# Kernel tuning notes

Measured on AMD Instinct MI355X. Metric: run time of the kernel, lower is better.

## Reference

```python
import jax, jax.numpy as jnp
import numpy as np

B, TC, TP = 2, 1024, 512
NVC, NVP = 8, 4
D, K, H, DFF, L, HOR, NQ = 128, 3, 8, 512, 2, 96, 3
DK = D // H
MASK_VAL = -1e4  # finite stand-in for -inf; entmax15 support never reaches entries this far below the row max


def entmax15(z):
    # Exact 1.5-entmax over the last axis (Peters & Martins sort-based algorithm).
    z = z / 2.0
    z = z - jnp.max(z, axis=-1, keepdims=True)
    zs = jnp.flip(jnp.sort(z, axis=-1), axis=-1)  # descending
    kk = jnp.arange(1, z.shape[-1] + 1, dtype=z.dtype)
    mean = jnp.cumsum(zs, axis=-1) / kk
    meansq = jnp.cumsum(zs * zs, axis=-1) / kk
    ss = kk * (meansq - mean * mean)
    delta = (1.0 - ss) / kk
    pos = delta > 0
    sqrt_d = jnp.where(pos, jnp.sqrt(jnp.where(pos, delta, 1.0)), 0.0)  # grad-safe sqrt
    tau = mean - sqrt_d
    support = jnp.sum((tau <= zs).astype(jnp.int32), axis=-1, keepdims=True)
    tau_star = jnp.take_along_axis(tau, support - 1, axis=-1)
    return jnp.square(jnp.clip(z - tau_star, 0.0, None))


def layer_norm(x, g, b, eps=1e-5):
    m = jnp.mean(x, axis=-1, keepdims=True)
    v = jnp.mean(jnp.square(x - m), axis=-1, keepdims=True)
    return (x - m) * jax.lax.rsqrt(v + eps) * g + b


def selector(x, conv_w, conv_b, sel_w, sel_b, key):
    # x: [B, T, nv]; causal depthwise-grouped conv -> per-var local states [B, T, nv, D]
    Bs, T, nv = x.shape
    xc = jnp.transpose(x, (0, 2, 1))  # [B, nv, T]
    out = jax.lax.conv_general_dilated(
        xc, conv_w, window_strides=(1,), padding=[(K - 1, 0)],
        dimension_numbers=('NCH', 'OIH', 'NCH'), feature_group_count=nv)
    ls = out.reshape(Bs, nv, D, T) + conv_b[None, :, :, None]
    ls = jnp.transpose(ls, (0, 3, 1, 2))  # [B, T, nv, D]
    scores = ls @ sel_w + sel_b  # [B, T, nv]
    scores = jnp.clip(scores, -10.0, 10.0)
    scores = scores + 1e-4 * jax.random.normal(key, scores.shape, scores.dtype)
    w = entmax15(scores)  # [B, T, nv]
    weighted = jnp.sum(ls * w[..., None], axis=2)  # [B, T, D]
    return weighted, w


def attn_block(x, Wq, bq, Wk, bk, Wv, bv, Wo, bo):
    Bs, T, _ = x.shape
    q = (x @ Wq + bq).reshape(Bs, T, H, DK)
    k = (x @ Wk + bk).reshape(Bs, T, H, DK)
    v = (x @ Wv + bv).reshape(Bs, T, H, DK)
    scores = jnp.einsum('bthd,bshd->bhts', q, k) / jnp.sqrt(jnp.float32(DK))
    mask = jnp.triu(jnp.ones((T, T), bool), 1)
    scores = jnp.where(mask[None, None], MASK_VAL, scores)
    w = entmax15(scores)            # [B, H, T, T]
    w_avg = jnp.mean(w, axis=1)     # [B, T, T]
    v_comb = jnp.mean(v, axis=2)    # [B, T, DK]
    out = jnp.einsum('bts,bsd->btd', w_avg, v_comb)
    return out @ Wo + bo, w_avg


def forward(x_cond, x_pred, cw_c, cb_c, sw_c, sb_c, cw_p, cb_p, sw_p, sb_p,
            Wq, bq, Wk, bk, Wv, bv, Wo, bo, ln1_g, ln1_b,
            fw1, fb1, fw2, fb2, ln2_g, ln2_b, proj_w, proj_b):
    nk = jax.random.key(42)
    xc, v_cond = selector(x_cond, cw_c, cb_c, sw_c, sb_c, jax.random.fold_in(nk, 0))
    xp, v_pred = selector(x_pred, cw_p, cb_p, sw_p, sb_p, jax.random.fold_in(nk, 1))
    x = jnp.concatenate([xc, xp], axis=1)  # [B, TC+TP, D]
    logs = []
    for l in range(L):
        a, w = attn_block(x, Wq[l], bq[l], Wk[l], bk[l], Wv[l], bv[l], Wo[l], bo[l])
        x = layer_norm(x + a, ln1_g[l], ln1_b[l])
        h = jax.nn.relu(x @ fw1[l] + fb1[l])
        x = layer_norm(h @ fw2[l] + fb2[l] + x, ln2_g[l], ln2_b[l])
        logs.append(w)
    seq_last = x[:, -1, :]
    out = jnp.einsum('bd,qdh->bqh', seq_last, proj_w) + proj_b  # [B, NQ, HOR]
    return out, v_cond, v_pred, jnp.stack(logs)


def setup_inputs():
    key = jax.random.key(0)
    ks = jax.random.split(key, 16)
    def w(i, shp):
        return (0.02 * jax.random.normal(ks[i], shp)).astype(jnp.float32)
    z = lambda shp: jnp.zeros(shp, jnp.float32)
    o = lambda shp: jnp.ones(shp, jnp.float32)
    return {
        'x_cond': jax.random.normal(ks[0], (B, TC, NVC), jnp.float32),
        'x_pred': jax.random.normal(ks[1], (B, TP, NVP), jnp.float32),
        'cw_c': w(2, (NVC * D, 1, K)), 'cb_c': z((NVC, D)),
        'sw_c': w(3, (D,)), 'sb_c': z((1,)),
        'cw_p': w(4, (NVP * D, 1, K)), 'cb_p': z((NVP, D)),
        'sw_p': w(5, (D,)), 'sb_p': z((1,)),
        'Wq': w(6, (L, D, D)), 'bq': z((L, D)),
        'Wk': w(7, (L, D, D)), 'bk': z((L, D)),
        'Wv': w(8, (L, D, D)), 'bv': z((L, D)),
        'Wo': w(9, (L, DK, D)), 'bo': z((L, D)),
        'ln1_g': o((L, D)), 'ln1_b': z((L, D)),
        'fw1': w(10, (L, D, DFF)), 'fb1': z((L, DFF)),
        'fw2': w(11, (L, DFF, D)), 'fb2': z((L, D)),
        'ln2_g': o((L, D)), 'ln2_b': z((L, D)),
        'proj_w': w(12, (NQ, D, HOR)), 'proj_b': z((NQ, HOR)),
    }


def reference(x_cond, x_pred, cw_c, cb_c, sw_c, sb_c, cw_p, cb_p, sw_p, sb_p,
              Wq, bq, Wk, bk, Wv, bv, Wo, bo, ln1_g, ln1_b,
              fw1, fb1, fw2, fb2, ln2_g, ln2_b, proj_w, proj_b):
    return forward(x_cond, x_pred, cw_c, cb_c, sw_c, sb_c, cw_p, cb_p, sw_p, sb_p,
                   Wq, bq, Wk, bk, Wv, bv, Wo, bo, ln1_g, ln1_b,
                   fw1, fb1, fw2, fb2, ln2_g, ln2_b, proj_w, proj_b)
```

## Files before the change

### kernel.cpp

```cpp
#include <hip/hip_runtime.h>

namespace {

constexpr int NB_  = 2;
constexpr int TC_  = 1024;
constexpr int TP_  = 512;
constexpr int TT_  = 1536;
constexpr int D_   = 128;
constexpr int H_   = 8;
constexpr int DK_  = 16;
constexpr int DFF_ = 512;
constexpr int L_   = 2;
constexpr int HOR_ = 96;
constexpr int NQ_  = 3;

constexpr int SCP_ = TT_ + 8;

typedef _Float16 h2 __attribute__((ext_vector_type(2)));

constexpr int OFF_OUT  = 0;
constexpr int OFF_VC   = NB_ * NQ_ * HOR_;
constexpr int OFF_VP   = OFF_VC + NB_ * TC_ * 8;
constexpr int OFF_LOGS = OFF_VP + NB_ * TP_ * 4;

constexpr int WS_XA  = 0;
constexpr int WS_XB  = WS_XA  + NB_ * TT_ * D_;
constexpr int WS_Q16 = WS_XB  + NB_ * TT_ * D_;
constexpr int WS_K16 = WS_Q16 + NB_ * TT_ * D_ / 2;
constexpr int WS_VC  = WS_K16 + NB_ * TT_ * D_ / 2;
constexpr int WS_WVC = WS_VC  + NB_ * TT_ * DK_;
constexpr int WS_BVC = WS_WVC + L_ * D_ * DK_;

__device__ inline float dot2f(h2 a, h2 b, float c) {
#if __has_builtin(__builtin_amdgcn_fdot2)
    return __builtin_amdgcn_fdot2(a, b, c, false);
#else
    return c + (float)a[0] * (float)b[0] + (float)a[1] * (float)b[1];
#endif
}

__device__ inline unsigned pack2h(float a, float b) {
#if __has_builtin(__builtin_amdgcn_cvt_pkrtz)
    return __builtin_bit_cast(unsigned, __builtin_amdgcn_cvt_pkrtz(a, b));
#else
    h2 p; p[0] = (_Float16)a; p[1] = (_Float16)b;
    return __builtin_bit_cast(unsigned, p);
#endif
}

__device__ inline float fast_rcp(float x) {
#if __has_builtin(__builtin_amdgcn_rcpf)
    return __builtin_amdgcn_rcpf(x);
#else
    return 1.0f / x;
#endif
}

template <int CTRL>
__device__ inline float dpp_add(float x) {
    const int y = __builtin_amdgcn_update_dpp(
        0, __builtin_bit_cast(int, x), CTRL, 0xF, 0xF, true);
    return x + __builtin_bit_cast(float, y);
}
template <int CTRL>
__device__ inline float dpp_maxf(float x) {
    const int y = __builtin_amdgcn_update_dpp(
        __builtin_bit_cast(int, x), __builtin_bit_cast(int, x),
        CTRL, 0xF, 0xF, false);
    return fmaxf(x, __builtin_bit_cast(float, y));
}
__device__ inline float bcast63(float x) {
    return __builtin_bit_cast(float,
        __builtin_amdgcn_readlane(__builtin_bit_cast(int, x), 63));
}
__device__ inline float wave_sum_l63(float x) {
    x = dpp_add<0x111>(x); x = dpp_add<0x112>(x); x = dpp_add<0x114>(x);
    x = dpp_add<0x118>(x); x = dpp_add<0x142>(x); x = dpp_add<0x143>(x);
    return x;
}
__device__ inline float wave_sum(float x) { return bcast63(wave_sum_l63(x)); }
__device__ inline float wave_max(float x) {
    x = dpp_maxf<0x111>(x); x = dpp_maxf<0x112>(x); x = dpp_maxf<0x114>(x);
    x = dpp_maxf<0x118>(x); x = dpp_maxf<0x142>(x); x = dpp_maxf<0x143>(x);
    return bcast63(x);
}

__global__ __launch_bounds__(128) void prep_wvc_kernel(
    const float* __restrict__ Wv, const float* __restrict__ bv,
    float* __restrict__ wvc, float* __restrict__ bvc)
{
    const int l = blockIdx.x;
    const float* W  = Wv + (long)l * D_ * D_;
    const float* bb = bv + l * D_;
    float* wv = wvc + l * D_ * DK_;
    float* bo = bvc + l * DK_;
    const int tid = threadIdx.x;
    for (int idx = tid; idx < D_ * DK_; idx += 128) {
        const int i = idx >> 4, dk = idx & 15;
        float s = 0.f;
        #pragma unroll
        for (int hh = 0; hh < H_; ++hh) s += W[i * D_ + hh * DK_ + dk];
        wv[idx] = s * 0.125f;
    }
    if (tid < DK_) {
        float s = 0.f;
        #pragma unroll
        for (int hh = 0; hh < H_; ++hh) s += bb[hh * DK_ + tid];
        bo[tid] = s * 0.125f;
    }
}

template <int NV>
__device__ inline void selector_qkv_body(
    const float* __restrict__ x, const float* __restrict__ cw,
    const float* __restrict__ cb, const float* __restrict__ sw,
    const float* __restrict__ sb, float* __restrict__ vout,
    float* __restrict__ xout, int Tsel, int row_off, int blk,
    const float* __restrict__ Wq, const float* __restrict__ bq,
    const float* __restrict__ Wk, const float* __restrict__ bk,
    const float* __restrict__ wvc, const float* __restrict__ bvc,
    _Float16* __restrict__ q16, _Float16* __restrict__ k16,
    float* __restrict__ vc)
{
    const int b = blk / Tsel;
    const int t = blk - b * Tsel;
    const int tid = threadIdx.x;
    const int d = tid & 127;
    const int hi = tid >> 7;
    const int lane = tid & 63, wave = tid >> 6;

    __shared__ float wsum[4][NV];
    __shared__ float wls[NV];
    __shared__ float xr[D_];
    __shared__ float vred[DK_][8];

    float xw[3 * NV];
    #pragma unroll
    for (int kk = 0; kk < 3; ++kk) {
        const int ts = t + kk - 2;
        #pragma unroll
        for (int v = 0; v < NV; ++v)
            xw[kk * NV + v] = (ts >= 0) ? x[((long)b * Tsel + ts) * NV + v] : 0.0f;
    }

    float ls[NV];
    #pragma unroll
    for (int v = 0; v < NV; ++v) {
        const float* cwp = cw + ((long)(v * D_ + d)) * 3;
        float a = cb[v * D_ + d];
        a = fmaf(xw[0 * NV + v], cwp[0], a);
        a = fmaf(xw[1 * NV + v], cwp[1], a);
        a = fmaf(xw[2 * NV + v], cwp[2], a);
        ls[v] = a;
    }

    {
        const float swd = sw[d];
        float p[NV];
        #pragma unroll
        for (int v = 0; v < NV; ++v) p[v] = ls[v] * swd;
        #pragma unroll
        for (int v = 0; v < NV; ++v) p[v] = wave_sum_l63(p[v]);
        if (lane == 63) {
            #pragma unroll
            for (int v = 0; v < NV; ++v) wsum[wave][v] = p[v];
        }
    }
    __syncthreads();

    if (tid == 0) {
        float u[NV];
        float m = -1e30f;
        #pragma unroll
        for (int v = 0; v < NV; ++v) {
            float s = wsum[0][v] + wsum[1][v] + sb[0];
            s = fminf(fmaxf(s, -10.0f), 10.0f);
            u[v] = 0.5f * s;
            m = fmaxf(m, u[v]);
        }
        float tau = m - 1.0f;
        for (int it = 0; it < 12; ++it) {
            float S1 = 0.f, S2 = 0.f;
            #pragma unroll
            for (int v = 0; v < NV; ++v) {
                float dd = fmaxf(u[v] - tau, 0.f);
                S1 += dd; S2 = fmaf(dd, dd, S2);
            }
            tau += (S2 - 1.0f) * 0.5f * fast_rcp(S1);
        }
        {
            float S1 = 0.f, S2 = 0.f, K = 0.f;
            #pragma unroll
            for (int v = 0; v < NV; ++v) {
                if (u[v] > tau) { S1 += u[v]; S2 = fmaf(u[v], u[v], S2); K += 1.f; }
            }
            const float mean = S1 / K;
            const float arg  = fmaxf(fmaf(mean, mean, -(S2 - 1.0f) / K), 0.f);
            tau = mean - sqrtf(arg);
        }
        #pragma unroll
        for (int v = 0; v < NV; ++v) {
            float dd = fmaxf(u[v] - tau, 0.f);
            wls[v] = dd * dd;
        }
    }
    __syncthreads();

    float acc = 0.f;
    #pragma unroll
    for (int v = 0; v < NV; ++v) acc = fmaf(ls[v], wls[v], acc);
    const long row = (long)b * TT_ + row_off + t;
    if (hi == 0) {
        xout[row * D_ + d] = acc;
        xr[d] = acc;
    }
    if (tid < NV) vout[((long)b * Tsel + t) * NV + tid] = wls[tid];
    __syncthreads();

    {
        const float* __restrict__ W = hi ? Wk : Wq;
        float a = hi ? bk[d] : bq[d];
        for (int i = 0; i < D_; ++i) a = fmaf(xr[i], W[i * D_ + d], a);
        _Float16* __restrict__ dst = hi ? k16 : q16;
        dst[row * D_ + d] = (_Float16)a;
    }

    if (tid < 128) {
        const int dk = tid & 15, ch = tid >> 4;
        float p = 0.f;
        #pragma unroll
        for (int i = 0; i < 16; ++i)
            p = fmaf(xr[ch * 16 + i], wvc[(ch * 16 + i) * DK_ + dk], p);
        vred[dk][ch] = p;
    }
    __syncthreads();
    if (tid < DK_) {
        float s = bvc[tid];
        #pragma unroll
        for (int ch = 0; ch < 8; ++ch) s += vred[tid][ch];
        vc[row * DK_ + tid] = s;
    }
}

__global__ __launch_bounds__(256) void pre_kernel(
    const float* __restrict__ x_cond, const float* __restrict__ cw_c,
    const float* __restrict__ cb_c, const float* __restrict__ sw_c,
    const float* __restrict__ sb_c,
    const float* __restrict__ x_pred, const float* __restrict__ cw_p,
    const float* __restrict__ cb_p, const float* __restrict__ sw_p,
    const float* __restrict__ sb_p,
    float* __restrict__ vc_out, float* __restrict__ vp_out,
    float* __restrict__ xout,
    const float* __restrict__ Wq, const float* __restrict__ bq,
    const float* __restrict__ Wk, const float* __restrict__ bk,
    const float* __restrict__ wvc, const float* __restrict__ bvc,
    _Float16* __restrict__ q16, _Float16* __restrict__ k16,
    float* __restrict__ vc)
{
    const int blk = blockIdx.x;
    if (blk < NB_ * TC_) {
        selector_qkv_body<8>(x_cond, cw_c, cb_c, sw_c, sb_c, vc_out, xout,
                             TC_, 0, blk, Wq, bq, Wk, bk, wvc, bvc,
                             q16, k16, vc);
    } else {
        selector_qkv_body<4>(x_pred, cw_p, cb_p, sw_p, sb_p, vp_out, xout,
                             TP_, TC_, blk - NB_ * TC_,
                             Wq, bq, Wk, bk, wvc, bvc, q16, k16, vc);
    }
}

template <int NJ>
__device__ inline void entmax_head2(unsigned short* __restrict__ sa,
                                    unsigned short* __restrict__ sb,
                                    int lane, int t)
{
    const unsigned* __restrict__ rpa = (const unsigned*)sa;
    const unsigned* __restrict__ rpb = (const unsigned*)sb;
    float va[2 * NJ], vb[2 * NJ];
    #pragma unroll
    for (int j = 0; j < NJ; ++j) {
        const unsigned dwa = rpa[64 * j + lane];
        const unsigned dwb = rpb[64 * j + lane];
        const h2 ha = __builtin_bit_cast(h2, dwa);
        const h2 hb = __builtin_bit_cast(h2, dwb);
        const int s0 = 128 * j + 2 * lane;
        const bool in0 = (s0 <= t), in1 = (s0 + 1 <= t);
        va[2*j]   = in0 ? (float)ha[0] : -1e30f;
        va[2*j+1] = in1 ? (float)ha[1] : -1e30f;
        vb[2*j]   = in0 ? (float)hb[0] : -1e30f;
        vb[2*j+1] = in1 ? (float)hb[1] : -1e30f;
    }

    float ma0 = va[0], ma1 = va[1], mb0 = vb[0], mb1 = vb[1];
    #pragma unroll
    for (int j = 2; j < 2 * NJ; j += 2) {
        ma0 = fmaxf(ma0, va[j]); ma1 = fmaxf(ma1, va[j+1]);
        mb0 = fmaxf(mb0, vb[j]); mb1 = fmaxf(mb1, vb[j+1]);
    }
    const float ma = wave_max(fmaxf(ma0, ma1));
    const float mb = wave_max(fmaxf(mb0, mb1));

    float ta = ma - 1.0f, tb = mb - 1.0f;
    #pragma unroll
    for (int it = 0; it < 7; ++it) {
        float a10 = 0.f, a11 = 0.f, a20 = 0.f, a21 = 0.f;
        float b10 = 0.f, b11 = 0.f, b20 = 0.f, b21 = 0.f;
        #pragma unroll
        for (int j = 0; j < 2 * NJ; j += 2) {
            const float da0 = fmaxf(va[j]   - ta, 0.f);
            const float da1 = fmaxf(va[j+1] - ta, 0.f);
            const float db0 = fmaxf(vb[j]   - tb, 0.f);
            const float db1 = fmaxf(vb[j+1] - tb, 0.f);
            a10 += da0; a11 += da1;
            a20 = fmaf(da0, da0, a20); a21 = fmaf(da1, da1, a21);
            b10 += db0; b11 += db1;
            b20 = fmaf(db0, db0, b20); b21 = fmaf(db1, db1, b21);
        }
        const float S1a = wave_sum(a10 + a11);
        const float S2a = wave_sum(a20 + a21);
        const float S1b = wave_sum(b10 + b11);
        const float S2b = wave_sum(b20 + b21);
        ta += (S2a - 1.0f) * 0.5f * fast_rcp(S1a);
        tb += (S2b - 1.0f) * 0.5f * fast_rcp(S1b);
    }
    {
        float a1 = 0.f, a2 = 0.f, ka = 0.f;
        float b1 = 0.f, b2 = 0.f, kb = 0.f;
        #pragma unroll
        for (int j = 0; j < 2 * NJ; ++j) {
            if (va[j] > ta) { a1 += va[j]; a2 = fmaf(va[j], va[j], a2); ka += 1.f; }
            if (vb[j] > tb) { b1 += vb[j]; b2 = fmaf(vb[j], vb[j], b2); kb += 1.f; }
        }
        a1 = wave_sum(a1); a2 = wave_sum(a2); ka = wave_sum(ka);
        b1 = wave_sum(b1); b2 = wave_sum(b2); kb = wave_sum(kb);
        const float meana = a1 / ka;
        const float arga  = fmaxf(fmaf(meana, meana, -(a2 - 1.0f) / ka), 0.f);
        ta = meana - sqrtf(arga);
        const float meanb = b1 / kb;
        const float argb  = fmaxf(fmaf(meanb, meanb, -(b2 - 1.0f) / kb), 0.f);
        tb = meanb - sqrtf(argb);
    }
    unsigned* __restrict__ wpa = (unsigned*)sa;
    unsigned* __restrict__ wpb = (unsigned*)sb;
    #pragma unroll
    for (int j = 0; j < NJ; ++j) {
        const float da0 = fmaxf(va[2*j]   - ta, 0.f);
        const float da1 = fmaxf(va[2*j+1] - ta, 0.f);
        const float db0 = fmaxf(vb[2*j]   - tb, 0.f);
        const float db1 = fmaxf(vb[2*j+1] - tb, 0.f);
        wpa[64 * j + lane] = pack2h(da0 * da0, da1 * da1);
        wpb[64 * j + lane] = pack2h(db0 * db0, db1 * db1);
    }
}

template <int NJ>
__device__ inline void entmax_pair(unsigned short* __restrict__ scb,
                                   int wave, int lane, int t)
{
    entmax_head2<NJ>(scb + (wave * 2 + 0) * SCP_,
                     scb + (wave * 2 + 1) * SCP_, lane, t);
}

__global__ __launch_bounds__(256) void attn_kernel(
    const _Float16* __restrict__ q16, const _Float16* __restrict__ k16,
    const float* __restrict__ vcomb, const float* __restrict__ xin,
    float* __restrict__ xout,
    const float* __restrict__ Wo, const float* __restrict__ bo,
    const float* __restrict__ lng, const float* __restrict__ lnb,
    float* __restrict__ logs)
{
    __shared__ unsigned short scb[H_ * SCP_];
    __shared__ _Float16 qrow16[D_];
    __shared__ float red[64];
    __shared__ float o16[DK_];
    __shared__ float yrow[D_];
    __shared__ float stat[2];

    const int blk = blockIdx.x;
    const int t = TT_ - 1 - (blk >> 1);
    const int b = blk & 1;
    const int tid = threadIdx.x;
    const int lane = tid & 63, wave = tid >> 6;
    const long rowq  = (long)b * TT_ + t;
    const long bbase = (long)b * TT_;

    if (tid < 64)
        ((unsigned*)qrow16)[tid] = ((const unsigned*)(q16 + rowq * D_))[tid];
    __syncthreads();

    {
        const int h  = tid & 7;
        const int sl = tid >> 3;
        unsigned short* __restrict__ srow = scb + h * SCP_;
        h2 qv[8];
        __builtin_memcpy(qv, (const _Float16*)qrow16 + h * DK_, 32);
        for (int s = sl; s <= t; s += 32) {
            float4 kk0, kk1;
            {
                const float4* kp4 = (const float4*)(k16 + (bbase + s) * D_ + h * DK_);
                kk0 = kp4[0]; kk1 = kp4[1];
            }
            h2 kh[8];
            __builtin_memcpy(kh,     &kk0, 16);
            __builtin_memcpy(kh + 4, &kk1, 16);
            float dot = 0.f;
            #pragma unroll
            for (int i2 = 0; i2 < 8; ++i2) dot = dot2f(qv[i2], kh[i2], dot);
            const _Float16 sh = (_Float16)(dot * 0.125f);
            srow[s] = __builtin_bit_cast(unsigned short, sh);
        }
    }
    __syncthreads();

    {
        const int njn = (t >> 7) + 1;
        switch ((njn + 1) & ~1) {
        case 2:  entmax_pair<2 >(scb, wave, lane, t); break;
        case 4:  entmax_pair<4 >(scb, wave, lane, t); break;
        case 6:  entmax_pair<6 >(scb, wave, lane, t); break;
        case 8:  entmax_pair<8 >(scb, wave, lane, t); break;
        case 10: entmax_pair<10>(scb, wave, lane, t); break;
        default: entmax_pair<12>(scb, wave, lane, t); break;
        }
    }
    __syncthreads();

    float4 A0 = make_float4(0,0,0,0), A1 = A0, A2 = A0, A3 = A0;
    float* lrow = logs + rowq * TT_;
    const unsigned* __restrict__ rp0 = (const unsigned*)scb;
    #pragma unroll
    for (int it = 0; it < 3; ++it) {
        const int dwi = tid + 256 * it;
        const int s0 = 2 * dwi;
        if (s0 <= t) {
            h2 hs = __builtin_bit_cast(h2, rp0[dwi]);
            #pragma unroll
            for (int h = 1; h < H_; ++h)
                hs = hs + __builtin_bit_cast(h2, rp0[h * (SCP_ / 2) + dwi]);
            const float wa0 = (float)hs[0] * 0.125f;
            const float wa1 = (float)hs[1] * 0.125f;
            {
                const float4* vp = (const float4*)(vcomb + (bbase + s0) * DK_);
                const float4 v0 = vp[0], v1 = vp[1], v2 = vp[2], v3 = vp[3];
                A0.x = fmaf(wa0, v0.x, A0.x); A0.y = fmaf(wa0, v0.y, A0.y);
                A0.z = fmaf(wa0, v0.z, A0.z); A0.w = fmaf(wa0, v0.w, A0.w);
                A1.x = fmaf(wa0, v1.x, A1.x); A1.y = fmaf(wa0, v1.y, A1.y);
                A1.z = fmaf(wa0, v1.z, A1.z); A1.w = fmaf(wa0, v1.w, A1.w);
                A2.x = fmaf(wa0, v2.x, A2.x); A2.y = fmaf(wa0, v2.y, A2.y);
                A2.z = fmaf(wa0, v2.z, A2.z); A2.w = fmaf(wa0, v2.w, A2.w);
                A3.x = fmaf(wa0, v3.x, A3.x); A3.y = fmaf(wa0, v3.y, A3.y);
                A3.z = fmaf(wa0, v3.z, A3.z); A3.w = fmaf(wa0, v3.w, A3.w);
            }
            if (s0 + 1 <= t) {
                const float4* vp = (const float4*)(vcomb + (bbase + s0 + 1) * DK_);
                const float4 v0 = vp[0], v1 = vp[1], v2 = vp[2], v3 = vp[3];
                A0.x = fmaf(wa1, v0.x, A0.x); A0.y = fmaf(wa1, v0.y, A0.y);
                A0.z = fmaf(wa1, v0.z, A0.z); A0.w = fmaf(wa1, v0.w, A0.w);
                A1.x = fmaf(wa1, v1.x, A1.x); A1.y = fmaf(wa1, v1.y, A1.y);
                A1.z = fmaf(wa1, v1.z, A1.z); A1.w = fmaf(wa1, v1.w, A1.w);
                A2.x = fmaf(wa1, v2.x, A2.x); A2.y = fmaf(wa1, v2.y, A2.y);
                A2.z = fmaf(wa1, v2.z, A2.z); A2.w = fmaf(wa1, v2.w, A2.w);
                A3.x = fmaf(wa1, v3.x, A3.x); A3.y = fmaf(wa1, v3.y, A3.y);
                A3.z = fmaf(wa1, v3.z, A3.z); A3.w = fmaf(wa1, v3.w, A3.w);
            }
            *(float2*)(lrow + s0) = make_float2(wa0, wa1);
        } else {
            *(float2*)(lrow + s0) = make_float2(0.f, 0.f);
        }
    }
    A0.x = wave_sum_l63(A0.x); A0.y = wave_sum_l63(A0.y);
    A0.z = wave_sum_l63(A0.z); A0.w = wave_sum_l63(A0.w);
    A1.x = wave_sum_l63(A1.x); A1.y = wave_sum_l63(A1.y);
    A1.z = wave_sum_l63(A1.z); A1.w = wave_sum_l63(A1.w);
    A2.x = wave_sum_l63(A2.x); A2.y = wave_sum_l63(A2.y);
    A2.z = wave_sum_l63(A2.z); A2.w = wave_sum_l63(A2.w);
    A3.x = wave_sum_l63(A3.x); A3.y = wave_sum_l63(A3.y);
    A3.z = wave_sum_l63(A3.z); A3.w = wave_sum_l63(A3.w);
    if (lane == 63) {
        float* r = red + wave * 16;
        r[0]=A0.x; r[1]=A0.y; r[2]=A0.z; r[3]=A0.w;
        r[4]=A1.x; r[5]=A1.y; r[6]=A1.z; r[7]=A1.w;
        r[8]=A2.x; r[9]=A2.y; r[10]=A2.z; r[11]=A2.w;
        r[12]=A3.x; r[13]=A3.y; r[14]=A3.z; r[15]=A3.w;
    }
    __syncthreads();
    if (tid < DK_) o16[tid] = red[tid] + red[16 + tid] + red[32 + tid] + red[48 + tid];
    __syncthreads();

    float y = 0.f;
    if (tid < D_) {
        float a = bo[tid];
        #pragma unroll
        for (int j = 0; j < DK_; ++j) a = fmaf(o16[j], Wo[j * D_ + tid], a);
        y = xin[rowq * D_ + tid] + a;
        yrow[tid] = y;
    }
    __syncthreads();
    if (tid < 64) {
        const float y0 = yrow[tid], y1 = yrow[tid + 64];
        float sm = wave_sum_l63(y0 + y1);
        float sq = wave_sum_l63(fmaf(y0, y0, y1 * y1));
        if (tid == 63) {
            const float mean = sm * (1.0f / D_);
            stat[0] = mean;
            stat[1] = fmaxf(sq * (1.0f / D_) - mean * mean, 0.f);
        }
    }
    __syncthreads();
    if (tid < D_) {
        const float r = rsqrtf(stat[1] + 1e-5f);
        xout[rowq * D_ + tid] = (y - stat[0]) * r * lng[tid] + lnb[tid];
    }
}

__global__ __launch_bounds__(256) void ffn_kernel(
    const float* __restrict__ xin, float* __restrict__ xout,
    const float* __restrict__ fw1, const float* __restrict__ fb1,
    const float* __restrict__ fw2, const float* __restrict__ fb2,
    const float* __restrict__ g, const float* __restrict__ bta,
    int do_qkv,
    const float* __restrict__ Wq, const float* __restrict__ bq,
    const float* __restrict__ Wk, const float* __restrict__ bk,
    const float* __restrict__ wvc, const float* __restrict__ bvc,
    _Float16* __restrict__ q16, _Float16* __restrict__ k16,
    float* __restrict__ vc,
    int do_proj, const float* __restrict__ pw,
    const float* __restrict__ pb, float* __restrict__ outp)
{
    __shared__ float xrT[D_][4];
    __shared__ float hbT[DFF_][4];
    __shared__ float pred[2][4][D_];
    __shared__ float yb[4][D_];
    __shared__ float xn[D_];

    const long row0 = (long)blockIdx.x * 4;
    const int tid = threadIdx.x;

    for (int idx = tid; idx < 4 * D_; idx += 256) {
        const int r = idx >> 7, i = idx & 127;
        xrT[i][r] = xin[row0 * D_ + idx];
    }
    __syncthreads();

    {
        const int c = tid;
        float4 a0 = make_float4(0,0,0,0), a1 = a0;
        for (int i = 0; i < D_; ++i) {
            const float w0 = fw1[i * DFF_ + c];
            const float w1 = fw1[i * DFF_ + c + 256];
            const float4 xv = *(const float4*)&xrT[i][0];
            a0.x = fmaf(xv.x, w0, a0.x); a0.y = fmaf(xv.y, w0, a0.y);
            a0.z = fmaf(xv.z, w0, a0.z); a0.w = fmaf(xv.w, w0, a0.w);
            a1.x = fmaf(xv.x, w1, a1.x); a1.y = fmaf(xv.y, w1, a1.y);
            a1.z = fmaf(xv.z, w1, a1.z); a1.w = fmaf(xv.w, w1, a1.w);
        }
        const float b0 = fb1[c], b1 = fb1[c + 256];
        float4 h0, h1;
        h0.x = fmaxf(a0.x + b0, 0.f); h0.y = fmaxf(a0.y + b0, 0.f);
        h0.z = fmaxf(a0.z + b0, 0.f); h0.w = fmaxf(a0.w + b0, 0.f);
        h1.x = fmaxf(a1.x + b1, 0.f); h1.y = fmaxf(a1.y + b1, 0.f);
        h1.z = fmaxf(a1.z + b1, 0.f); h1.w = fmaxf(a1.w + b1, 0.f);
        *(float4*)&hbT[c][0]       = h0;
        *(float4*)&hbT[c + 256][0] = h1;
    }
    __syncthreads();

    {
        const int d = tid & 127;
        const int half = tid >> 7;
        const int j0 = half * 256;
        float a0 = 0.f, a1 = 0.f, a2 = 0.f, a3 = 0.f;
        for (int j = j0; j < j0 + 256; ++j) {
            const float wv = fw2[j * D_ + d];
            const float4 hv = *(const float4*)&hbT[j][0];
            a0 = fmaf(hv.x, wv, a0);
            a1 = fmaf(hv.y, wv, a1);
            a2 = fmaf(hv.z, wv, a2);
            a3 = fmaf(hv.w, wv, a3);
        }
        pred[half][0][d] = a0; pred[half][1][d] = a1;
        pred[half][2][d] = a2; pred[half][3][d] = a3;
    }
    __syncthreads();

    {
        const int d = tid & 127;
        const int r0 = (tid >> 7) * 2;
        const float bb = fb2[d];
        yb[r0 + 0][d] = pred[0][r0 + 0][d] + pred[1][r0 + 0][d] + bb + xrT[d][r0 + 0];
        yb[r0 + 1][d] = pred[0][r0 + 1][d] + pred[1][r0 + 1][d] + bb + xrT[d][r0 + 1];
    }
    __syncthreads();

    const int w = tid >> 6, lane = tid & 63;
    const bool pblk = do_proj && (((row0 + 4) % TT_) == 0);
    {
        const float y0 = yb[w][lane], y1 = yb[w][lane + 64];
        const float sm = wave_sum(y0 + y1);
        const float sq = wave_sum(fmaf(y0, y0, y1 * y1));
        const float mean = sm * (1.0f / D_);
        const float var  = fmaxf(sq * (1.0f / D_) - mean * mean, 0.f);
        const float rcp = rsqrtf(var + 1e-5f);
        const float o0 = (y0 - mean) * rcp * g[lane]      + bta[lane];
        const float o1 = (y1 - mean) * rcp * g[lane + 64] + bta[lane + 64];
        xout[(row0 + w) * D_ + lane]      = o0;
        xout[(row0 + w) * D_ + lane + 64] = o1;
        xrT[lane][w]      = o0;
        xrT[lane + 64][w] = o1;
        if (pblk && w == 3) { xn[lane] = o0; xn[lane + 64] = o1; }
    }

    if (do_qkv) {
        __syncthreads();
        const int c = tid & 127;
        const int which = tid >> 7;
        const float* __restrict__ W = which ? Wk : Wq;
        const float bb = which ? bk[c] : bq[c];
        float a0 = bb, a1 = bb, a2 = bb, a3 = bb;
        for (int i = 0; i < D_; ++i) {
            const float wv = W[i * D_ + c];
            const float4 xv = *(const float4*)&xrT[i][0];
            a0 = fmaf(xv.x, wv, a0);
            a1 = fmaf(xv.y, wv, a1);
            a2 = fmaf(xv.z, wv, a2);
            a3 = fmaf(xv.w, wv, a3);
        }
        _Float16* __restrict__ dst = which ? k16 : q16;
        dst[(row0 + 0) * D_ + c] = (_Float16)a0;
        dst[(row0 + 1) * D_ + c] = (_Float16)a1;
        dst[(row0 + 2) * D_ + c] = (_Float16)a2;
        dst[(row0 + 3) * D_ + c] = (_Float16)a3;

        if (tid < 64) {
            const int r = tid >> 4, c16 = tid & 15;
            float av = bvc[c16];
            for (int i = 0; i < D_; ++i)
                av = fmaf(xrT[i][r], wvc[i * DK_ + c16], av);
            vc[(row0 + r) * DK_ + c16] = av;
        }
    }

    if (pblk) {
        __syncthreads();
        const int b = (int)((row0 + 3) / TT_);
        for (int idx = tid; idx < NQ_ * HOR_; idx += 256) {
            const int qq = idx / HOR_, hh = idx - qq * HOR_;
            float s = pb[idx];
            for (int d = 0; d < D_; ++d)
                s = fmaf(xn[d], pw[((long)qq * D_ + d) * HOR_ + hh], s);
            outp[b * NQ_ * HOR_ + idx] = s;
        }
    }
}

}

extern "C" void kernel_launch(void* const* d_in, const int* in_sizes, int n_in,
                              void* d_out, int out_size, void* d_ws, size_t ws_size,
                              hipStream_t stream) {
    (void)in_sizes; (void)n_in; (void)out_size; (void)ws_size;

    const float* x_cond = (const float*)d_in[0];
    const float* x_pred = (const float*)d_in[1];
    const float* cw_c   = (const float*)d_in[2];
    const float* cb_c   = (const float*)d_in[3];
    const float* sw_c   = (const float*)d_in[4];
    const float* sb_c   = (const float*)d_in[5];
    const float* cw_p   = (const float*)d_in[6];
    const float* cb_p   = (const float*)d_in[7];
    const float* sw_p   = (const float*)d_in[8];
    const float* sb_p   = (const float*)d_in[9];
    const float* Wq     = (const float*)d_in[10];
    const float* bq     = (const float*)d_in[11];
    const float* Wk     = (const float*)d_in[12];
    const float* bk     = (const float*)d_in[13];
    const float* Wv     = (const float*)d_in[14];
    const float* bv     = (const float*)d_in[15];
    const float* Wo     = (const float*)d_in[16];
    const float* bo     = (const float*)d_in[17];
    const float* ln1g   = (const float*)d_in[18];
    const float* ln1b   = (const float*)d_in[19];
    const float* fw1    = (const float*)d_in[20];
    const float* fb1    = (const float*)d_in[21];
    const float* fw2    = (const float*)d_in[22];
    const float* fb2    = (const float*)d_in[23];
    const float* ln2g   = (const float*)d_in[24];
    const float* ln2b   = (const float*)d_in[25];
    const float* pw     = (const float*)d_in[26];
    const float* pb     = (const float*)d_in[27];

    float* outp = (float*)d_out;
    float* ws   = (float*)d_ws;
    float*     xA   = ws + WS_XA;
    float*     xB   = ws + WS_XB;
    _Float16*  q16  = (_Float16*)(ws + WS_Q16);
    _Float16*  k16  = (_Float16*)(ws + WS_K16);
    float*     vcb  = ws + WS_VC;
    float*     wvc  = ws + WS_WVC;
    float*     bvc  = ws + WS_BVC;

    prep_wvc_kernel<<<L_, 128, 0, stream>>>(Wv, bv, wvc, bvc);

    pre_kernel<<<NB_ * TC_ + NB_ * TP_, 256, 0, stream>>>(
        x_cond, cw_c, cb_c, sw_c, sb_c,
        x_pred, cw_p, cb_p, sw_p, sb_p,
        outp + OFF_VC, outp + OFF_VP, xA,
        Wq, bq, Wk, bk, wvc, bvc, q16, k16, vcb);

    for (int l = 0; l < L_; ++l) {
        attn_kernel<<<NB_ * TT_, 256, 0, stream>>>(
            q16, k16, vcb, xA, xB,
            Wo + (long)l * DK_ * D_, bo + l * D_,
            ln1g + l * D_, ln1b + l * D_,
            outp + OFF_LOGS + (long)l * NB_ * TT_ * TT_);
        const int nl = l + 1;
        ffn_kernel<<<NB_ * TT_ / 4, 256, 0, stream>>>(
            xB, xA, fw1 + (long)l * D_ * DFF_, fb1 + l * DFF_,
            fw2 + (long)l * DFF_ * D_, fb2 + l * D_,
            ln2g + l * D_, ln2b + l * D_,
            (l < L_ - 1) ? 1 : 0,
            Wq + (long)nl * D_ * D_ * (l < L_ - 1),
            bq + nl * D_ * (l < L_ - 1),
            Wk + (long)nl * D_ * D_ * (l < L_ - 1),
            bk + nl * D_ * (l < L_ - 1),
            wvc + nl * D_ * DK_ * (l < L_ - 1),
            bvc + nl * DK_ * (l < L_ - 1),
            q16, k16, vcb,
            (l == L_ - 1) ? 1 : 0, pw, pb, outp);
    }
}
```

Before: 309.1 us.

## Process four timesteps per block in selector+QKV pre-kernel

Restructures the pre-kernel so each 256-thread block handles four timesteps, one per wavefront. The selector scores and entmax are now computed per wave with wave-wide reductions, removing several block-level syncs and the single-thread entmax. The Q/K projection reuses each weight load across four rows, cutting global weight traffic fourfold. The trade-off is a quarter as many blocks and a V projection that runs on one wave only. A trivial reordering of two reductions in the attention kernel is also included.

```diff
diff --git a/kernel.cpp b/kernel.cpp
--- a/kernel.cpp
+++ b/kernel.cpp
@@ -122,18 +122,16 @@
     _Float16* __restrict__ q16, _Float16* __restrict__ k16,
     float* __restrict__ vc)
 {
-    const int b = blk / Tsel;
-    const int t = blk - b * Tsel;
+    const int tpb = Tsel / 4;
+    const int b   = blk / tpb;
+    const int t0  = (blk - b * tpb) * 4;
     const int tid = threadIdx.x;
-    const int d = tid & 127;
-    const int hi = tid >> 7;
     const int lane = tid & 63, wave = tid >> 6;
-
-    __shared__ float wsum[4][NV];
-    __shared__ float wls[NV];
-    __shared__ float xr[D_];
-    __shared__ float vred[DK_][8];
-
+    const int t = t0 + wave;
+
+    __shared__ float xrT[D_][4];
+
+    const int d0 = lane, d1 = lane + 64;
     float xw[3 * NV];
     #pragma unroll
     for (int kk = 0; kk < 3; ++kk) {
@@ -142,38 +140,30 @@
         for (int v = 0; v < NV; ++v)
             xw[kk * NV + v] = (ts >= 0) ? x[((long)b * Tsel + ts) * NV + v] : 0.0f;
     }
-
-    float ls[NV];
+    float ls0[NV], ls1[NV];
     #pragma unroll
     for (int v = 0; v < NV; ++v) {
-        const float* cwp = cw + ((long)(v * D_ + d)) * 3;
-        float a = cb[v * D_ + d];
-        a = fmaf(xw[0 * NV + v], cwp[0], a);
-        a = fmaf(xw[1 * NV + v], cwp[1], a);
-        a = fmaf(xw[2 * NV + v], cwp[2], a);
-        ls[v] = a;
-    }
-
-    {
-        const float swd = sw[d];
-        float p[NV];
-        #pragma unroll
-        for (int v = 0; v < NV; ++v) p[v] = ls[v] * swd;
-        #pragma unroll
-        for (int v = 0; v < NV; ++v) p[v] = wave_sum_l63(p[v]);
-        if (lane == 63) {
-            #pragma unroll
-            for (int v = 0; v < NV; ++v) wsum[wave][v] = p[v];
-        }
-    }
-    __syncthreads();
-
-    if (tid == 0) {
-        float u[NV];
+        const float* c0 = cw + ((long)(v * D_ + d0)) * 3;
+        const float* c1 = cw + ((long)(v * D_ + d1)) * 3;
+        float a0 = cb[v * D_ + d0], a1 = cb[v * D_ + d1];
+        a0 = fmaf(xw[0*NV+v], c0[0], a0); a1 = fmaf(xw[0*NV+v], c1[0], a1);
+        a0 = fmaf(xw[1*NV+v], c0[1], a0); a1 = fmaf(xw[1*NV+v], c1[1], a1);
+        a0 = fmaf(xw[2*NV+v], c0[2], a0); a1 = fmaf(xw[2*NV+v], c1[2], a1);
+        ls0[v] = a0; ls1[v] = a1;
+    }
+    float u[NV];
+    {
+        const float s0 = sw[d0], s1 = sw[d1];
+        #pragma unroll
+        for (int v = 0; v < NV; ++v)
+            u[v] = wave_sum(fmaf(ls1[v], s1, ls0[v] * s0));
+    }
+    float wls[NV];
+    {
         float m = -1e30f;
         #pragma unroll
         for (int v = 0; v < NV; ++v) {
-            float s = wsum[0][v] + wsum[1][v] + sb[0];
+            float s = u[v] + sb[0];
             s = fminf(fmaxf(s, -10.0f), 10.0f);
             u[v] = 0.5f * s;
             m = fmaxf(m, u[v]);
@@ -188,57 +178,65 @@
             }
             tau += (S2 - 1.0f) * 0.5f * fast_rcp(S1);
         }
-        {
-            float S1 = 0.f, S2 = 0.f, K = 0.f;
-            #pragma unroll
-            for (int v = 0; v < NV; ++v) {
-                if (u[v] > tau) { S1 += u[v]; S2 = fmaf(u[v], u[v], S2); K += 1.f; }
-            }
-            const float mean = S1 / K;
-            const float arg  = fmaxf(fmaf(mean, mean, -(S2 - 1.0f) / K), 0.f);
-            tau = mean - sqrtf(arg);
-        }
+        float S1 = 0.f, S2 = 0.f, K = 0.f;
         #pragma unroll
         for (int v = 0; v < NV; ++v) {
-            float dd = fmaxf(u[v] - tau, 0.f);
+            if (u[v] > tau) { S1 += u[v]; S2 = fmaf(u[v], u[v], S2); K += 1.f; }
+        }
+        const float mean = S1 / K;
+        const float arg  = fmaxf(fmaf(mean, mean, -(S2 - 1.0f) / K), 0.f);
+        tau = mean - sqrtf(arg);
+        #pragma unroll
+        for (int v = 0; v < NV; ++v) {
+            const float dd = fmaxf(u[v] - tau, 0.f);
             wls[v] = dd * dd;
         }
     }
-    __syncthreads();
-
-    float acc = 0.f;
+    float acc0 = 0.f, acc1 = 0.f;
     #pragma unroll
-    for (int v = 0; v < NV; ++v) acc = fmaf(ls[v], wls[v], acc);
-    const long row = (long)b * TT_ + row_off + t;
-    if (hi == 0) {
-        xout[row * D_ + d] = acc;
-        xr[d] = acc;
-    }
-    if (tid < NV) vout[((long)b * Tsel + t) * NV + tid] = wls[tid];
-    __syncthreads();
-
-    {
-        const float* __restrict__ W = hi ? Wk : Wq;
-        float a = hi ? bk[d] : bq[d];
-        for (int i = 0; i < D_; ++i) a = fmaf(xr[i], W[i * D_ + d], a);
-        _Float16* __restrict__ dst = hi ? k16 : q16;
-        dst[row * D_ + d] = (_Float16)a;
-    }
-
-    if (tid < 128) {
-        const int dk = tid & 15, ch = tid >> 4;
-        float p = 0.f;
-        #pragma unroll
-        for (int i = 0; i < 16; ++i)
-            p = fmaf(xr[ch * 16 + i], wvc[(ch * 16 + i) * DK_ + dk], p);
-        vred[dk][ch] = p;
-    }
-    __syncthreads();
-    if (tid < DK_) {
-        float s = bvc[tid];
-        #pragma unroll
-        for (int ch = 0; ch < 8; ++ch) s += vred[tid][ch];
-        vc[row * DK_ + tid] = s;
+    for (int v = 0; v < NV; ++v) {
+        acc0 = fmaf(ls0[v], wls[v], acc0);
+        acc1 = fmaf(ls1[v], wls[v], acc1);
+    }
+    const long rowb = (long)b * TT_ + row_off + t0;
+    const long row  = rowb + wave;
+    xout[row * D_ + d0] = acc0;
+    xout[row * D_ + d1] = acc1;
+    xrT[d0][wave] = acc0;
+    xrT[d1][wave] = acc1;
+    if (lane == 0) {
+        #pragma unroll
+        for (int v = 0; v < NV; ++v)
+            vout[((long)b * Tsel + t) * NV + v] = wls[v];
+    }
+    __syncthreads();
+
+    {
+        const int c = tid & 127;
+        const int which = tid >> 7;
+        const float* __restrict__ W = which ? Wk : Wq;
+        const float bb = which ? bk[c] : bq[c];
+        float a0 = bb, a1 = bb, a2 = bb, a3 = bb;
+        for (int i = 0; i < D_; ++i) {
+            const float wv = W[i * D_ + c];
+            const float4 xv = *(const float4*)&xrT[i][0];
+            a0 = fmaf(xv.x, wv, a0);
+            a1 = fmaf(xv.y, wv, a1);
+            a2 = fmaf(xv.z, wv, a2);
+            a3 = fmaf(xv.w, wv, a3);
+        }
+        _Float16* __restrict__ dst = which ? k16 : q16;
+        dst[(rowb + 0) * D_ + c] = (_Float16)a0;
+        dst[(rowb + 1) * D_ + c] = (_Float16)a1;
+        dst[(rowb + 2) * D_ + c] = (_Float16)a2;
+        dst[(rowb + 3) * D_ + c] = (_Float16)a3;
+    }
+    if (tid < 64) {
+        const int r = tid >> 4, c16 = tid & 15;
+        float av = bvc[c16];
+        for (int i = 0; i < D_; ++i)
+            av = fmaf(xrT[i][r], wvc[i * DK_ + c16], av);
+        vc[(rowb + r) * DK_ + c16] = av;
     }
 }
 
@@ -258,13 +256,13 @@
     float* __restrict__ vc)
 {
     const int blk = blockIdx.x;
-    if (blk < NB_ * TC_) {
+    if (blk < NB_ * TC_ / 4) {
         selector_qkv_body<8>(x_cond, cw_c, cb_c, sw_c, sb_c, vc_out, xout,
                              TC_, 0, blk, Wq, bq, Wk, bk, wvc, bvc,
                              q16, k16, vc);
     } else {
         selector_qkv_body<4>(x_pred, cw_p, cb_p, sw_p, sb_p, vp_out, xout,
-                             TP_, TC_, blk - NB_ * TC_,
+                             TP_, TC_, blk - NB_ * TC_ / 4,
                              Wq, bq, Wk, bk, wvc, bvc, q16, k16, vc);
     }
 }
@@ -475,7 +473,7 @@
     A2.x = wave_sum_l63(A2.x); A2.y = wave_sum_l63(A2.y);
     A2.z = wave_sum_l63(A2.z); A2.w = wave_sum_l63(A2.w);
     A3.x = wave_sum_l63(A3.x); A3.y = wave_sum_l63(A3.y);
-    A3.z = wave_sum_l63(A3.z); A3.w = wave_sum_l63(A3.w);
+    A3.w = wave_sum_l63(A3.w); A3.z = wave_sum_l63(A3.z);
     if (lane == 63) {
         float* r = red + wave * 16;
         r[0]=A0.x; r[1]=A0.y; r[2]=A0.z; r[3]=A0.w;
@@ -701,7 +699,7 @@
 
     prep_wvc_kernel<<<L_, 128, 0, stream>>>(Wv, bv, wvc, bvc);
 
-    pre_kernel<<<NB_ * TC_ + NB_ * TP_, 256, 0, stream>>>(
+    pre_kernel<<<(NB_ * TC_ + NB_ * TP_) / 4, 256, 0, stream>>>(
         x_cond, cw_c, cb_c, sw_c, sb_c,
         x_pred, cw_p, cb_p, sw_p, sb_p,
         outp + OFF_VC, outp + OFF_VP, xA,
```

After: 300.2 us. 2.9% less time.
